# Kernel tuning notes

Hardware: AMD Instinct MI355X
Metric: run time of the kernel (lower is better)

The kernel has to match this reference:

```python
import jax, jax.numpy as jnp
import numpy as np

D = 8    # embedding dim
H = 4    # heads
E = 4    # dim per head (dim_heads=4)
NL = 4   # axial attention layers
B, S, IM = 4, 20, 64


def _axis_attn(xt, wq, wkv, wo, bo, axis):
    # xt: (b, s, h, w, d); self-attention along `axis` in {1,2,3}
    z = jnp.moveaxis(xt, axis, 3)                      # (..., L, d)
    q = z @ wq                                          # (..., L, H*E)
    kv = z @ wkv
    k, v = kv[..., :H * E], kv[..., H * E:]
    sh = q.shape[:-1]
    q = q.reshape(*sh, H, E)
    k = k.reshape(*sh, H, E)
    v = v.reshape(*sh, H, E)
    dots = jnp.einsum('...ihe,...jhe->...hij', q, k) * (E ** -0.5)
    attn = jax.nn.softmax(dots, axis=-1)
    o = jnp.einsum('...hij,...jhe->...ihe', attn, v).reshape(*sh, H * E)
    o = o @ wo + bo                                     # (..., L, d)
    return jnp.moveaxis(o, 3, axis)


def setup_inputs() -> dict:
    key = jax.random.key(0)
    ks = jax.random.split(key, 12)
    x = jax.random.normal(ks[0], (B, S, 1, IM, IM), jnp.float32)
    conv_w = jax.random.normal(ks[1], (D,), jnp.float32) * 0.5        # 1x1 conv, bias=False
    pos_s = jax.random.normal(ks[2], (1, S, D, 1, 1), jnp.float32) * 0.02
    pos_h = jax.random.normal(ks[3], (1, 1, D, IM, 1), jnp.float32) * 0.02
    pos_w = jax.random.normal(ks[4], (1, 1, D, 1, IM), jnp.float32) * 0.02
    Wq = jax.random.normal(ks[5], (NL, 3, D, H * E), jnp.float32) / np.sqrt(D).astype(np.float32)
    Wkv = jax.random.normal(ks[6], (NL, 3, D, 2 * H * E), jnp.float32) / np.sqrt(D).astype(np.float32)
    Wo = jax.random.normal(ks[7], (NL, 3, H * E, D), jnp.float32) / np.sqrt(H * E).astype(np.float32)
    bo = jnp.zeros((NL, 3, D), jnp.float32)
    Wc = jax.random.normal(ks[8], (1, D * IM * IM), jnp.float32) * 0.01
    bc = jnp.zeros((1,), jnp.float32)
    return {"x": x, "conv_w": conv_w, "pos_s": pos_s, "pos_h": pos_h, "pos_w": pos_w,
            "Wq": Wq, "Wkv": Wkv, "Wo": Wo, "bo": bo, "Wc": Wc, "bc": bc}


def reference(x, conv_w, pos_s, pos_h, pos_w, Wq, Wkv, Wo, bo, Wc, bc):
    b = x.shape[0]
    # 1x1 conv (1 -> D, no bias) + ReLU; input channel dim is 1 so it's a broadcast scale
    emb = jax.nn.relu(x * conv_w[None, None, :, None, None])   # (b, s, D, h, w)
    # additive axial positional embedding
    emb = emb + pos_s + pos_h + pos_w
    xt = jnp.moveaxis(emb, 2, -1)                              # (b, s, h, w, D)
    z = xt
    for l in range(NL):  # dropout(p=0.1) between layers is identity in eval mode
        z = sum(_axis_attn(z, Wq[l, a], Wkv[l, a], Wo[l, a], bo[l, a], a + 1)
                for a in range(3))
    z = z + xt                                                 # outer residual
    z = jnp.max(z, axis=1)                                     # max over s -> (b, h, w, D)
    flat = jnp.moveaxis(z, -1, 1).reshape(b, -1)               # torch flatten order (D, h, w)
    return jax.nn.sigmoid(flat @ Wc.T + bc)                    # (b, 1)
```

## Files before the change

kernel.cpp:

```cpp
#include <hip/hip_runtime.h>
#include <math.h>

#define DD 8
#define HH 4
#define EE 4
#define NLAYER 4
#define BB 4
#define SS 20
#define IMM 64

static constexpr int NPOS = BB * SS * IMM * IMM;
static constexpr size_t ZBYTES = (size_t)NPOS * DD * 4;

__global__ __launch_bounds__(256)
void emb_kernel(const float* __restrict__ x, const float* __restrict__ conv_w,
                const float* __restrict__ pos_s, const float* __restrict__ pos_h,
                const float* __restrict__ pos_w, float* __restrict__ xt) {
    int idx = blockIdx.x * 256 + threadIdx.x;
    if (idx >= NPOS) return;
    int j = idx & 63;
    int i = (idx >> 6) & 63;
    int s = (idx >> 12) % SS;
    float xv = x[idx];
    float o[8];
#pragma unroll
    for (int d = 0; d < 8; ++d) {
        float v = xv * conv_w[d];
        v = v > 0.f ? v : 0.f;
        o[d] = v + pos_s[s * 8 + d] + pos_h[d * 64 + i] + pos_w[d * 64 + j];
    }
    float4* dst = (float4*)(xt + (size_t)idx * 8);
    dst[0] = make_float4(o[0], o[1], o[2], o[3]);
    dst[1] = make_float4(o[4], o[5], o[6], o[7]);
}

__device__ __forceinline__ float dot4(float4 a, float4 b) {
    return fmaf(a.w, b.w, fmaf(a.z, b.z, fmaf(a.y, b.y, a.x * b.x)));
}
__device__ __forceinline__ float dot4i(float4 a, float4 b, float c0) {
    return fmaf(a.x, b.x, fmaf(a.y, b.y, fmaf(a.z, b.z, fmaf(a.w, b.w, c0))));
}

template <int L, int RPT, int LINES, bool ACCUM, int STG, int WPE>
__global__ __launch_bounds__(HH * (L / RPT) * LINES, WPE)
void attn_kernel(const float* __restrict__ src, float* __restrict__ dst,
                 const float* __restrict__ Wq, const float* __restrict__ Wkv,
                 const float* __restrict__ Wo, const float* __restrict__ bo,
                 int m0, int c1, int m1, int stride) {
    constexpr int RG = L / RPT;
    constexpr int TL = HH * RG;
    constexpr int NT = TL * LINES;
    constexpr int LL = L * LINES;

    __shared__ float4 zl4[2][LL];
    __shared__ float4 kv4[LL][8];
    __shared__ float4 olT4[HH][LL];
    __shared__ float4 wq4[8][4];
    __shared__ float4 wkv4[8][8];
    __shared__ float4 woq4[16][2];
    __shared__ float4 bo4_s[2];
    __shared__ float  Mh2[LINES][HH];

    const int t = threadIdx.x;
    if (t < 32) wq4[t >> 2][t & 3]  = *(const float4*)(Wq  + t * 4);
    if (t < 64) wkv4[t >> 3][t & 7] = *(const float4*)(Wkv + t * 4);
    if (t < 32) woq4[t >> 1][t & 1] = *(const float4*)(Wo  + t * 4);
    if (t < 2)  bo4_s[t]            = *(const float4*)(bo  + t * 4);
    if (t < LINES * HH) Mh2[t / HH][t % HH] = 0.f;

    auto line_base = [&](int ln) -> size_t {
        int lid = blockIdx.x * LINES + ln;
        int u0 = lid & 63;
        int rest = lid >> 6;
        int u1 = rest % c1;
        int b  = rest / c1;
        return (size_t)b * 655360 + (size_t)u1 * m1 + (size_t)u0 * m0;
    };

    for (int idx = t; idx < LL * 2; idx += NT) {
        int q, ln, p;
        if (STG == 1) { q = idx & 1; int r = idx >> 1; ln = r % LINES; p = r / LINES; }
        else          { q = idx & 1; int r = idx >> 1; ln = r / L;     p = r % L;     }
        zl4[q][ln * L + p] = *(const float4*)(src + line_base(ln) + (size_t)p * stride + q * 4);
    }
    __syncthreads();

    {
        const int c = t & 7;
        float4 wc[8];
#pragma unroll
        for (int d = 0; d < 8; ++d) wc[d] = wkv4[d][c];
        for (int idx = t; idx < LL * 8; idx += NT) {
            int lp = idx >> 3;
            float4 z0 = zl4[0][lp], z1 = zl4[1][lp];
            const float zs[8] = {z0.x, z0.y, z0.z, z0.w, z1.x, z1.y, z1.z, z1.w};
            float4 acc = make_float4(0.f, 0.f, 0.f, 0.f);
#pragma unroll
            for (int d = 0; d < 8; ++d) {
                acc.x += zs[d] * wc[d].x; acc.y += zs[d] * wc[d].y;
                acc.z += zs[d] * wc[d].z; acc.w += zs[d] * wc[d].w;
            }
            kv4[lp][c] = acc;
            if (c < 4)
                atomicMax((int*)&Mh2[lp / L][c], __float_as_int(dot4(acc, acc)));
        }
    }
    __syncthreads();

    {
        const int ln = t / TL;
        const int r  = t % TL;
        const int h  = r / RG;
        const int rg = r % RG;
        const int jb = ln * L;
        const int i0 = rg * RPT;
        const float SC = 0.5f * 1.44269504f;

        float4 q[RPT];
        float nB2[RPT];
        const float mh2 = Mh2[ln][h];
#pragma unroll
        for (int k = 0; k < RPT; ++k) {
            float4 z0 = zl4[0][jb + i0 + k], z1 = zl4[1][jb + i0 + k];
            const float zs[8] = {z0.x, z0.y, z0.z, z0.w, z1.x, z1.y, z1.z, z1.w};
            float4 acc = make_float4(0.f, 0.f, 0.f, 0.f);
#pragma unroll
            for (int d = 0; d < 8; ++d) {
                float4 w = wq4[d][h];
                acc.x += zs[d] * w.x; acc.y += zs[d] * w.y;
                acc.z += zs[d] * w.z; acc.w += zs[d] * w.w;
            }
            q[k] = make_float4(acc.x * SC, acc.y * SC, acc.z * SC, acc.w * SC);
            nB2[k] = -sqrtf(dot4(q[k], q[k]) * mh2);
        }

        float s[RPT];
        float4 o[RPT];
#pragma unroll
        for (int k = 0; k < RPT; ++k) { s[k] = 0.f; o[k] = make_float4(0.f, 0.f, 0.f, 0.f); }
#pragma unroll 4
        for (int j = 0; j < L; ++j) {
            float4 kk = kv4[jb + j][h];
            float4 vv = kv4[jb + j][4 + h];
#pragma unroll
            for (int k = 0; k < RPT; ++k) {
                float p = __builtin_amdgcn_exp2f(dot4i(q[k], kk, nB2[k]));
                s[k] += p;
                o[k].x += p * vv.x; o[k].y += p * vv.y;
                o[k].z += p * vv.z; o[k].w += p * vv.w;
            }
        }
#pragma unroll
        for (int k = 0; k < RPT; ++k) {
            const float inv = 1.f / fmaxf(s[k], 1e-37f);
            olT4[h][jb + i0 + k] =
                make_float4(o[k].x * inv, o[k].y * inv, o[k].z * inv, o[k].w * inv);
        }
    }
    __syncthreads();

    {
        const int dq = t & 1;
        float4 wr[16];
#pragma unroll
        for (int c = 0; c < 16; ++c) wr[c] = woq4[c][dq];
        float4 bo4 = bo4_s[dq];
        for (int idx = t; idx < LL * 2; idx += NT) {
            int ln, p;
            if (STG == 1) { int r = idx >> 1; ln = r % LINES; p = r / LINES; }
            else          { int r = idx >> 1; ln = r / L;     p = r % L;     }
            int lp = ln * L + p;
            float4 o0 = olT4[0][lp], o1 = olT4[1][lp];
            float4 o2 = olT4[2][lp], o3 = olT4[3][lp];
            const float oc[16] = {o0.x, o0.y, o0.z, o0.w, o1.x, o1.y, o1.z, o1.w,
                                  o2.x, o2.y, o2.z, o2.w, o3.x, o3.y, o3.z, o3.w};
            float4 acc = bo4;
#pragma unroll
            for (int c = 0; c < 16; ++c) {
                acc.x += oc[c] * wr[c].x; acc.y += oc[c] * wr[c].y;
                acc.z += oc[c] * wr[c].z; acc.w += oc[c] * wr[c].w;
            }
            float* gp = dst + line_base(ln) + (size_t)p * stride + dq * 4;
            if (ACCUM) {
                float4 old = *(const float4*)gp;
                acc.x += old.x; acc.y += old.y; acc.z += old.z; acc.w += old.w;
            }
            *(float4*)gp = acc;
        }
    }
}

__global__ __launch_bounds__(256)
void reduce_kernel(const float* __restrict__ z, const float* __restrict__ xt,
                   const float* __restrict__ Wc, float* __restrict__ accum) {
    const int b  = blockIdx.x >> 4;
    const int ij = ((blockIdx.x & 15) << 8) + threadIdx.x;
    float4 m0 = make_float4(-1e30f, -1e30f, -1e30f, -1e30f);
    float4 m1 = m0;
    for (int s = 0; s < SS; ++s) {
        size_t off = (((size_t)(b * SS + s)) * 4096 + ij) * 8;
        float4 a0 = *(const float4*)(z + off);
        float4 a1 = *(const float4*)(z + off + 4);
        float4 c0 = *(const float4*)(xt + off);
        float4 c1 = *(const float4*)(xt + off + 4);
        m0.x = fmaxf(m0.x, a0.x + c0.x); m0.y = fmaxf(m0.y, a0.y + c0.y);
        m0.z = fmaxf(m0.z, a0.z + c0.z); m0.w = fmaxf(m0.w, a0.w + c0.w);
        m1.x = fmaxf(m1.x, a1.x + c1.x); m1.y = fmaxf(m1.y, a1.y + c1.y);
        m1.z = fmaxf(m1.z, a1.z + c1.z); m1.w = fmaxf(m1.w, a1.w + c1.w);
    }
    float partial =
        m0.x * Wc[0 * 4096 + ij] + m0.y * Wc[1 * 4096 + ij] +
        m0.z * Wc[2 * 4096 + ij] + m0.w * Wc[3 * 4096 + ij] +
        m1.x * Wc[4 * 4096 + ij] + m1.y * Wc[5 * 4096 + ij] +
        m1.z * Wc[6 * 4096 + ij] + m1.w * Wc[7 * 4096 + ij];

    __shared__ float red[256];
    red[threadIdx.x] = partial;
    __syncthreads();
#pragma unroll
    for (int off = 128; off > 0; off >>= 1) {
        if (threadIdx.x < off) red[threadIdx.x] += red[threadIdx.x + off];
        __syncthreads();
    }
    if (threadIdx.x == 0) atomicAdd(&accum[b], red[0]);
}

__global__ void final_kernel(const float* __restrict__ accum,
                             const float* __restrict__ bc,
                             float* __restrict__ out) {
    int b = threadIdx.x;
    if (b < BB) out[b] = 1.f / (1.f + expf(-(accum[b] + bc[0])));
}

extern "C" void kernel_launch(void* const* d_in, const int* in_sizes, int n_in,
                              void* d_out, int out_size, void* d_ws, size_t ws_size,
                              hipStream_t stream) {
    const float* x      = (const float*)d_in[0];
    const float* conv_w = (const float*)d_in[1];
    const float* pos_s  = (const float*)d_in[2];
    const float* pos_h  = (const float*)d_in[3];
    const float* pos_w  = (const float*)d_in[4];
    const float* Wq     = (const float*)d_in[5];
    const float* Wkv    = (const float*)d_in[6];
    const float* Wo     = (const float*)d_in[7];
    const float* bo     = (const float*)d_in[8];
    const float* Wc     = (const float*)d_in[9];
    const float* bc     = (const float*)d_in[10];
    float* out = (float*)d_out;

    char* ws = (char*)d_ws;
    float* xt    = (float*)(ws);
    float* zA    = (float*)(ws + ZBYTES);
    float* zB    = (float*)(ws + 2 * ZBYTES);
    float* accum = (float*)(ws + 3 * ZBYTES);

    emb_kernel<<<NPOS / 256, 256, 0, stream>>>(x, conv_w, pos_s, pos_h, pos_w, xt);

    const float* cur = xt;
    float* bufs[2] = {zA, zB};
    int w = 0;
    for (int l = 0; l < NLAYER; ++l) {
        float* dstp = bufs[w];
        const float* wq0  = Wq  + (size_t)(l * 3 + 0) * 128;
        const float* wkv0 = Wkv + (size_t)(l * 3 + 0) * 256;
        const float* wo0  = Wo  + (size_t)(l * 3 + 0) * 128;
        const float* bo0  = bo  + (size_t)(l * 3 + 0) * 8;
        attn_kernel<SS, 2, 8, false, 1, 8><<<BB * IMM * IMM / 8, HH * (SS / 2) * 8, 0, stream>>>(
            cur, dstp, wq0, wkv0, wo0, bo0, 8, 64, 512, 32768);
        attn_kernel<IMM, 4, 2, true, 1, 4><<<BB * SS * IMM / 2, HH * (IMM / 4) * 2, 0, stream>>>(
            cur, dstp, wq0 + 128, wkv0 + 256, wo0 + 128, bo0 + 8, 8, 20, 32768, 512);
        attn_kernel<IMM, 4, 2, true, 0, 4><<<BB * SS * IMM / 2, HH * (IMM / 4) * 2, 0, stream>>>(
            cur, dstp, wq0 + 256, wkv0 + 512, wo0 + 256, bo0 + 16, 512, 20, 32768, 8);
        cur = dstp;
        w ^= 1;
    }

    hipMemsetAsync(accum, 0, BB * sizeof(float), stream);
    reduce_kernel<<<BB * 16, 256, 0, stream>>>(cur, xt, Wc, accum);
    final_kernel<<<1, 64, 0, stream>>>(accum, bc, out);
}
```

Measured before the change: 488.8 us.

## Alias z and output LDS buffers, prefetch residual, halve rows per thread

The z staging buffer and the per-head attention output buffer now share one LDS pool, with an extra barrier so the z reads finish before the outputs overwrite it. This shrinks shared memory per block. For the two length-64 axes, each thread now handles 2 query rows instead of 4, which doubles the threads per block, and the occupancy hint is raised to 8. Each thread's first residual value from dst is loaded early, alongside the staging loads, so its latency is hidden, and the key loop unroll goes from 4 to 8. The cost is an added barrier plus more threads re-reading K/V from LDS.

```diff
diff --git a/kernel.cpp b/kernel.cpp
--- a/kernel.cpp
+++ b/kernel.cpp
@@ -52,14 +52,16 @@
     constexpr int NT = TL * LINES;
     constexpr int LL = L * LINES;
 
-    __shared__ float4 zl4[2][LL];
+    __shared__ float4 pool4[HH * LL];
     __shared__ float4 kv4[LL][8];
-    __shared__ float4 olT4[HH][LL];
     __shared__ float4 wq4[8][4];
     __shared__ float4 wkv4[8][8];
     __shared__ float4 woq4[16][2];
     __shared__ float4 bo4_s[2];
     __shared__ float  Mh2[LINES][HH];
+
+#define ZL4(qq, lp)  pool4[(qq) * LL + (lp)]
+#define OLT4(hh, lp) pool4[(hh) * LL + (lp)]
 
     const int t = threadIdx.x;
     if (t < 32) wq4[t >> 2][t & 3]  = *(const float4*)(Wq  + t * 4);
@@ -76,12 +78,24 @@
         int b  = rest / c1;
         return (size_t)b * 655360 + (size_t)u1 * m1 + (size_t)u0 * m0;
     };
+    auto map_lp = [&](int idx, int& ln, int& p) {
+        int r = idx >> 1;
+        if (STG == 1) { ln = r % LINES; p = r / LINES; }
+        else          { ln = r / L;     p = r % L;     }
+    };
 
     for (int idx = t; idx < LL * 2; idx += NT) {
-        int q, ln, p;
-        if (STG == 1) { q = idx & 1; int r = idx >> 1; ln = r % LINES; p = r / LINES; }
-        else          { q = idx & 1; int r = idx >> 1; ln = r / L;     p = r % L;     }
-        zl4[q][ln * L + p] = *(const float4*)(src + line_base(ln) + (size_t)p * stride + q * 4);
+        int ln, p;
+        map_lp(idx, ln, p);
+        ZL4(idx & 1, ln * L + p) =
+            *(const float4*)(src + line_base(ln) + (size_t)p * stride + (idx & 1) * 4);
+    }
+
+    float4 dst_old = make_float4(0.f, 0.f, 0.f, 0.f);
+    if (ACCUM && t < LL * 2) {
+        int ln, p;
+        map_lp(t, ln, p);
+        dst_old = *(const float4*)(dst + line_base(ln) + (size_t)p * stride + (t & 1) * 4);
     }
     __syncthreads();
 
@@ -92,7 +106,7 @@
         for (int d = 0; d < 8; ++d) wc[d] = wkv4[d][c];
         for (int idx = t; idx < LL * 8; idx += NT) {
             int lp = idx >> 3;
-            float4 z0 = zl4[0][lp], z1 = zl4[1][lp];
+            float4 z0 = ZL4(0, lp), z1 = ZL4(1, lp);
             const float zs[8] = {z0.x, z0.y, z0.z, z0.w, z1.x, z1.y, z1.z, z1.w};
             float4 acc = make_float4(0.f, 0.f, 0.f, 0.f);
 #pragma unroll
@@ -121,7 +135,7 @@
         const float mh2 = Mh2[ln][h];
 #pragma unroll
         for (int k = 0; k < RPT; ++k) {
-            float4 z0 = zl4[0][jb + i0 + k], z1 = zl4[1][jb + i0 + k];
+            float4 z0 = ZL4(0, jb + i0 + k), z1 = ZL4(1, jb + i0 + k);
             const float zs[8] = {z0.x, z0.y, z0.z, z0.w, z1.x, z1.y, z1.z, z1.w};
             float4 acc = make_float4(0.f, 0.f, 0.f, 0.f);
 #pragma unroll
@@ -134,11 +148,13 @@
             nB2[k] = -sqrtf(dot4(q[k], q[k]) * mh2);
         }
 
+        __syncthreads();
+
         float s[RPT];
         float4 o[RPT];
 #pragma unroll
         for (int k = 0; k < RPT; ++k) { s[k] = 0.f; o[k] = make_float4(0.f, 0.f, 0.f, 0.f); }
-#pragma unroll 4
+#pragma unroll 8
         for (int j = 0; j < L; ++j) {
             float4 kk = kv4[jb + j][h];
             float4 vv = kv4[jb + j][4 + h];
@@ -153,7 +169,7 @@
 #pragma unroll
         for (int k = 0; k < RPT; ++k) {
             const float inv = 1.f / fmaxf(s[k], 1e-37f);
-            olT4[h][jb + i0 + k] =
+            OLT4(h, jb + i0 + k) =
                 make_float4(o[k].x * inv, o[k].y * inv, o[k].z * inv, o[k].w * inv);
         }
     }
@@ -167,11 +183,10 @@
         float4 bo4 = bo4_s[dq];
         for (int idx = t; idx < LL * 2; idx += NT) {
             int ln, p;
-            if (STG == 1) { int r = idx >> 1; ln = r % LINES; p = r / LINES; }
-            else          { int r = idx >> 1; ln = r / L;     p = r % L;     }
+            map_lp(idx, ln, p);
             int lp = ln * L + p;
-            float4 o0 = olT4[0][lp], o1 = olT4[1][lp];
-            float4 o2 = olT4[2][lp], o3 = olT4[3][lp];
+            float4 o0 = OLT4(0, lp), o1 = OLT4(1, lp);
+            float4 o2 = OLT4(2, lp), o3 = OLT4(3, lp);
             const float oc[16] = {o0.x, o0.y, o0.z, o0.w, o1.x, o1.y, o1.z, o1.w,
                                   o2.x, o2.y, o2.z, o2.w, o3.x, o3.y, o3.z, o3.w};
             float4 acc = bo4;
@@ -180,14 +195,20 @@
                 acc.x += oc[c] * wr[c].x; acc.y += oc[c] * wr[c].y;
                 acc.z += oc[c] * wr[c].z; acc.w += oc[c] * wr[c].w;
             }
-            float* gp = dst + line_base(ln) + (size_t)p * stride + dq * 4;
             if (ACCUM) {
-                float4 old = *(const float4*)gp;
-                acc.x += old.x; acc.y += old.y; acc.z += old.z; acc.w += old.w;
-            }
-            *(float4*)gp = acc;
-        }
-    }
+                if (idx == t) {
+                    acc.x += dst_old.x; acc.y += dst_old.y;
+                    acc.z += dst_old.z; acc.w += dst_old.w;
+                } else {
+                    float4 old = *(const float4*)(dst + line_base(ln) + (size_t)p * stride + dq * 4);
+                    acc.x += old.x; acc.y += old.y; acc.z += old.z; acc.w += old.w;
+                }
+            }
+            *(float4*)(dst + line_base(ln) + (size_t)p * stride + dq * 4) = acc;
+        }
+    }
+#undef ZL4
+#undef OLT4
 }
 
 __global__ __launch_bounds__(256)
@@ -267,9 +288,9 @@
         const float* bo0  = bo  + (size_t)(l * 3 + 0) * 8;
         attn_kernel<SS, 2, 8, false, 1, 8><<<BB * IMM * IMM / 8, HH * (SS / 2) * 8, 0, stream>>>(
             cur, dstp, wq0, wkv0, wo0, bo0, 8, 64, 512, 32768);
-        attn_kernel<IMM, 4, 2, true, 1, 4><<<BB * SS * IMM / 2, HH * (IMM / 4) * 2, 0, stream>>>(
+        attn_kernel<IMM, 2, 2, true, 1, 8><<<BB * SS * IMM / 2, HH * (IMM / 2) * 2, 0, stream>>>(
             cur, dstp, wq0 + 128, wkv0 + 256, wo0 + 128, bo0 + 8, 8, 20, 32768, 512);
-        attn_kernel<IMM, 4, 2, true, 0, 4><<<BB * SS * IMM / 2, HH * (IMM / 4) * 2, 0, stream>>>(
+        attn_kernel<IMM, 2, 2, true, 0, 8><<<BB * SS * IMM / 2, HH * (IMM / 2) * 2, 0, stream>>>(
             cur, dstp, wq0 + 256, wkv0 + 512, wo0 + 256, bo0 + 16, 512, 20, 32768, 8);
         cur = dstp;
         w ^= 1;
```

Result: faster. 455.7 us (-6.8%).
